# Kernel optimization log

Hardware: AMD Instinct MI355X
Metric: run time of the kernel (lower is better)

## Reference

```python
import math
import jax, jax.numpy as jnp
import numpy as np

N_HEAD = 16
HEAD_DIM = 128


def _rope(x, cos, sin):
    # x: (B,T,H,D); cos,sin: (T,1,D/2) broadcast over B,H
    d = x.shape[-1] // 2
    x1, x2 = x[..., :d], x[..., d:]
    return jnp.concatenate([x1 * cos + x2 * sin, -x1 * sin + x2 * cos], axis=-1)


def _rms_norm(x, eps=1e-6):
    return x * jax.lax.rsqrt(jnp.mean(x * x, axis=-1, keepdims=True) + eps)


def setup_inputs() -> dict:
    key = jax.random.key(0)
    ks = jax.random.split(key, 9)
    B, T, C = 2, 2048, 2048
    scale = 1.0 / math.sqrt(C)
    return {
        "x": jax.random.normal(ks[0], (B, T, C), jnp.float32),
        "ve": jax.random.normal(ks[1], (B, T, C), jnp.float32),
        "Wq": jax.random.normal(ks[2], (C, C), jnp.float32) * scale,
        "Wk": jax.random.normal(ks[3], (C, C), jnp.float32) * scale,
        "Wv": jax.random.normal(ks[4], (C, C), jnp.float32) * scale,
        "Wproj": jax.random.normal(ks[5], (C, C), jnp.float32) * scale,
        "Wgate": jax.random.normal(ks[6], (N_HEAD, 12), jnp.float32) * (1.0 / math.sqrt(12.0)),
        "cos": jax.random.uniform(ks[7], (T, 1, HEAD_DIM // 2), jnp.float32),
        "sin": jax.random.uniform(ks[8], (T, 1, HEAD_DIM // 2), jnp.float32),
        "window_left": 1024,
    }


def reference(x, ve, Wq, Wk, Wv, Wproj, Wgate, cos, sin, window_left):
    B, T, C = x.shape
    H, D = N_HEAD, HEAD_DIM

    # Linear projections (torch Linear: x @ W.T)
    q = (x @ Wq.T).reshape(B, T, H, D)
    k = (x @ Wk.T).reshape(B, T, H, D)
    v = (x @ Wv.T).reshape(B, T, H, D)

    # value-embedding gating (has_ve layer)
    gate = 3.0 * jax.nn.sigmoid(x[..., :12] @ Wgate.T)  # (B,T,H)
    v = v + gate[..., None] * ve.reshape(B, T, H, D)

    # rope + qk rms-norm * 1.2
    q = _rms_norm(_rope(q, cos, sin)) * 1.2
    k = _rms_norm(_rope(k, cos, sin)) * 1.2

    # windowed causal mask
    row = jnp.arange(T)[:, None]
    col = jnp.arange(T)[None, :]
    mask = row >= col
    if 0 < window_left < T:
        mask = mask & (row - col <= window_left)
    bias = jnp.where(mask, 0.0, -1e9).astype(x.dtype)  # (T,T)

    scale = 1.0 / math.sqrt(D)
    att = jnp.einsum("bqhd,bkhd->bhqk", q, k) * scale + bias[None, None]
    att = jax.nn.softmax(att, axis=-1)
    y = jnp.einsum("bhqk,bkhd->bqhd", att, v).reshape(B, T, H * D)
    return y @ Wproj.T
```

## Files before the change

### kernel.cpp

```cpp
#include <hip/hip_runtime.h>
#include <hip/hip_bf16.h>
#include <cstdint>

#define N_HEAD 16
#define HEAD_DIM 128

typedef __bf16 bf16;
typedef __bf16 bf16x8 __attribute__((ext_vector_type(8)));
typedef __bf16 bf16x4 __attribute__((ext_vector_type(4)));
typedef float f32x4 __attribute__((ext_vector_type(4)));

__device__ __forceinline__ void gload_lds16(const void* g, void* l) {
  auto gp = reinterpret_cast<const __attribute__((address_space(1))) char*>(
      reinterpret_cast<uintptr_t>(g));
  auto lp = reinterpret_cast<__attribute__((address_space(3))) char*>(
      reinterpret_cast<uintptr_t>(l));
  __builtin_amdgcn_global_load_lds(gp, lp, 16, 0, 0);
}

__global__ __launch_bounds__(256) void cvt_all(
    const float* __restrict__ x, const float* __restrict__ Wq,
    const float* __restrict__ Wk, const float* __restrict__ Wv,
    const float* __restrict__ Wp, bf16* __restrict__ xb,
    bf16* __restrict__ wqkv, bf16* __restrict__ wpb, int nx4, int nw4) {
  const int z = blockIdx.z;
  const float* in;
  bf16* out;
  int n4;
  if (z == 0)      { in = x;  out = xb;  n4 = nx4; }
  else if (z == 1) { in = Wq; out = wqkv;                     n4 = nw4; }
  else if (z == 2) { in = Wk; out = wqkv + (size_t)nw4 * 4;   n4 = nw4; }
  else if (z == 3) { in = Wv; out = wqkv + (size_t)nw4 * 8;   n4 = nw4; }
  else             { in = Wp; out = wpb;  n4 = nw4; }
  const int i = blockIdx.x * 256 + threadIdx.x;
  if (i >= n4) return;
  const float4 f = reinterpret_cast<const float4*>(in)[i];
  bf16x4 o;
  o.x = (bf16)f.x; o.y = (bf16)f.y; o.z = (bf16)f.z; o.w = (bf16)f.w;
  reinterpret_cast<bf16x4*>(out)[i] = o;
}

__global__ __launch_bounds__(512, 2) void gemm256(
    const bf16* __restrict__ A, const bf16* __restrict__ Bt,
    bf16* __restrict__ C, int M, int N, int K) {
  __shared__ __align__(16) char sA[2][32768];
  __shared__ __align__(16) char sB[2][32768];

  const int nwgy = M >> 8;
  const int nwg = gridDim.x;
  const int q8 = nwg >> 3;
  const int wgid = (blockIdx.x & 7) * q8 + (blockIdx.x >> 3);
  const int by = wgid % nwgy;
  const int bx = wgid / nwgy;

  const int tid = threadIdx.x;
  const int lane = tid & 63;
  const int wave = tid >> 6;
  const int wm = (wave >> 2) << 7;
  const int wn = (wave & 3) << 6;
  const int lr = lane & 15;
  const int lk16 = (lane >> 4) << 4;
  const int sx = (lr & 7) << 4;

  const bf16* Ab = A + (size_t)by * 256 * K;
  const bf16* Bb = Bt + (size_t)bx * 256 * K;

  int srow[2], scol[2];
#pragma unroll
  for (int pp = 0; pp < 2; ++pp) {
    const int o = pp * 8192 + tid * 16;
    srow[pp] = o >> 7;
    scol[pp] = (o & 127) ^ ((srow[pp] & 7) << 4);
  }

  auto stageA = [&](int buf, int half, int k0) {
#pragma unroll
    for (int pp = 0; pp < 2; ++pp)
      gload_lds16(Ab + (size_t)(half * 128 + srow[pp]) * K + k0 + (scol[pp] >> 1),
                  sA[buf] + half * 16384 + pp * 8192 + tid * 16);
  };
  auto stageB = [&](int buf, int half, int k0) {
#pragma unroll
    for (int pp = 0; pp < 2; ++pp)
      gload_lds16(Bb + (size_t)(half * 128 + srow[pp]) * K + k0 + (scol[pp] >> 1),
                  sB[buf] + half * 16384 + pp * 8192 + tid * 16);
  };

  f32x4 acc[8][4] = {};
  bf16x8 bF[4][2];

#define VMCNT4                                             \
  asm volatile("s_waitcnt vmcnt(4)" ::: "memory");         \
  __builtin_amdgcn_sched_barrier(0)
#define VMCNT0                                             \
  asm volatile("s_waitcnt vmcnt(0)" ::: "memory");         \
  __builtin_amdgcn_sched_barrier(0)

#define PHASE(BUF, P, STAGE, WAIT)                                             \
  {                                                                            \
    bf16x8 aF[2][2];                                                           \
    if (P == 0) {                                                              \
      _Pragma("unroll") for (int n = 0; n < 4; ++n)                            \
      _Pragma("unroll") for (int ks = 0; ks < 2; ++ks)                         \
        bF[n][ks] = *reinterpret_cast<const bf16x8*>(                          \
            sB[BUF] + (wn + n * 16 + lr) * 128 + ((ks * 64 + lk16) ^ sx));     \
    }                                                                          \
    _Pragma("unroll") for (int mi = 0; mi < 2; ++mi)                           \
    _Pragma("unroll") for (int ks = 0; ks < 2; ++ks)                           \
      aF[mi][ks] = *reinterpret_cast<const bf16x8*>(                           \
          sA[BUF] + (wm + (P * 2 + mi) * 16 + lr) * 128 +                      \
          ((ks * 64 + lk16) ^ sx));                                            \
    STAGE;                                                                     \
    WAIT;                                                                      \
    __builtin_amdgcn_s_barrier();                                              \
    __builtin_amdgcn_s_setprio(1);                                             \
    _Pragma("unroll") for (int ks = 0; ks < 2; ++ks)                           \
    _Pragma("unroll") for (int mi = 0; mi < 2; ++mi)                           \
    _Pragma("unroll") for (int n = 0; n < 4; ++n)                              \
      acc[P * 2 + mi][n] = __builtin_amdgcn_mfma_f32_16x16x32_bf16(            \
          aF[mi][ks], bF[n][ks], acc[P * 2 + mi][n], 0, 0, 0);                 \
    __builtin_amdgcn_s_setprio(0);                                             \
    __builtin_amdgcn_s_barrier();                                              \
  }

  const int nIt = K >> 7;

  stageB(0, 0, 0); stageB(0, 1, 0);
  stageA(0, 0, 0); stageA(0, 1, 0);
  stageB(1, 0, 64); stageB(1, 1, 64);
  VMCNT4;
  __builtin_amdgcn_s_barrier();

  int k0 = 0;
  for (int it = 0; it < nIt - 1; ++it, k0 += 128) {
    PHASE(0, 0, stageA(1, 0, k0 + 64), );
    PHASE(0, 1, stageA(1, 1, k0 + 64), );
    PHASE(0, 2, stageB(0, 0, k0 + 128), );
    PHASE(0, 3, stageB(0, 1, k0 + 128), VMCNT4);
    PHASE(1, 0, stageA(0, 0, k0 + 128), );
    PHASE(1, 1, stageA(0, 1, k0 + 128), );
    PHASE(1, 2, stageB(1, 0, k0 + 192), );
    PHASE(1, 3, stageB(1, 1, k0 + 192), VMCNT4);
  }
  PHASE(0, 0, stageA(1, 0, k0 + 64), );
  PHASE(0, 1, stageA(1, 1, k0 + 64), );
  PHASE(0, 2, , );
  PHASE(0, 3, , VMCNT0);
  PHASE(1, 0, , );
  PHASE(1, 1, , );
  PHASE(1, 2, , );
  PHASE(1, 3, , );
#undef PHASE
#undef VMCNT4
#undef VMCNT0

  const int orow = by * 256 + wm + (lane >> 4) * 4;
  const int ocol = bx * 256 + wn + lr;
#pragma unroll
  for (int m = 0; m < 8; ++m)
#pragma unroll
    for (int n = 0; n < 4; ++n)
#pragma unroll
      for (int r = 0; r < 4; ++r)
        C[(size_t)(orow + m * 16 + r) * N + (ocol + n * 16)] = (bf16)acc[m][n][r];
}

template <typename OutT>
__global__ __launch_bounds__(512, 2) void gemm128(
    const bf16* __restrict__ A, const bf16* __restrict__ Bt,
    OutT* __restrict__ C, int M, int Ncols, int K, int nOff) {
  __shared__ __align__(16) char sA[2][16384];
  __shared__ __align__(16) char sB[2][32768];

  const int nwgy = M >> 7;
  const int nwg = gridDim.x;
  const int q8 = nwg >> 3;
  const int wgid = (blockIdx.x & 7) * q8 + (blockIdx.x >> 3);
  const int by = wgid % nwgy;
  const int bx = wgid / nwgy;

  const int tid = threadIdx.x;
  const int lane = tid & 63;
  const int wave = tid >> 6;
  const int wn = wave << 5;
  const int lr = lane & 15;
  const int lk16 = (lane >> 4) << 4;
  const int sx = (lr & 7) << 4;

  const bf16* Ab = A + (size_t)by * 128 * K;
  const bf16* Bb = Bt + (size_t)(nOff + bx * 256) * K;

  int srow[2], scol[2];
#pragma unroll
  for (int pp = 0; pp < 2; ++pp) {
    const int o = pp * 8192 + tid * 16;
    srow[pp] = o >> 7;
    scol[pp] = (o & 127) ^ ((srow[pp] & 7) << 4);
  }

  auto stageB = [&](int buf, int half, int k0) {
#pragma unroll
    for (int pp = 0; pp < 2; ++pp)
      gload_lds16(Bb + (size_t)(half * 128 + srow[pp]) * K + k0 + (scol[pp] >> 1),
                  sB[buf] + half * 16384 + pp * 8192 + tid * 16);
  };
  auto stageA = [&](int buf, int half, int k0) {
    const int o = tid * 16;
    const int row = o >> 7;
    const int col = (o & 127) ^ ((row & 7) << 4);
    gload_lds16(Ab + (size_t)(half * 64 + row) * K + k0 + (col >> 1),
                sA[buf] + half * 8192 + o);
  };

  f32x4 acc[8][2] = {};
  bf16x8 bF[2][2];

#define WAITV(n)                                               \
  asm volatile("s_waitcnt vmcnt(" #n ")" ::: "memory");        \
  __builtin_amdgcn_sched_barrier(0)

#define PH128(BUF, P, STAGE, WAIT)                                             \
  {                                                                            \
    bf16x8 aF[2][2];                                                           \
    if (P == 0) {                                                              \
      _Pragma("unroll") for (int n = 0; n < 2; ++n)                            \
      _Pragma("unroll") for (int ks = 0; ks < 2; ++ks)                         \
        bF[n][ks] = *reinterpret_cast<const bf16x8*>(                          \
            sB[BUF] + (wn + n * 16 + lr) * 128 + ((ks * 64 + lk16) ^ sx));     \
    }                                                                          \
    _Pragma("unroll") for (int mi = 0; mi < 2; ++mi)                           \
    _Pragma("unroll") for (int ks = 0; ks < 2; ++ks)                           \
      aF[mi][ks] = *reinterpret_cast<const bf16x8*>(                           \
          sA[BUF] + ((P * 2 + mi) * 16 + lr) * 128 + ((ks * 64 + lk16) ^ sx)); \
    STAGE;                                                                     \
    WAIT;                                                                      \
    __builtin_amdgcn_s_barrier();                                              \
    __builtin_amdgcn_s_setprio(1);                                             \
    _Pragma("unroll") for (int ks = 0; ks < 2; ++ks)                           \
    _Pragma("unroll") for (int mi = 0; mi < 2; ++mi)                           \
    _Pragma("unroll") for (int n = 0; n < 2; ++n)                              \
      acc[P * 2 + mi][n] = __builtin_amdgcn_mfma_f32_16x16x32_bf16(            \
          aF[mi][ks], bF[n][ks], acc[P * 2 + mi][n], 0, 0, 0);                 \
    __builtin_amdgcn_s_setprio(0);                                             \
    __builtin_amdgcn_s_barrier();                                              \
  }

  const int nIt = K >> 7;

  stageB(0, 0, 0); stageB(0, 1, 0);
  stageA(0, 0, 0); stageA(0, 1, 0);
  stageB(1, 0, 64); stageB(1, 1, 64);
  stageA(1, 0, 64);
  WAITV(5);
  __builtin_amdgcn_s_barrier();

  int k0 = 0;
  for (int it = 0; it < nIt - 1; ++it, k0 += 128) {
    PH128(0, 0, stageA(1, 1, k0 + 64), );
    PH128(0, 1, stageB(0, 0, k0 + 128), WAITV(8));
    PH128(0, 2, (stageB(0, 1, k0 + 128), stageA(0, 0, k0 + 128)), );
    PH128(0, 3, , WAITV(6));
    PH128(1, 0, stageA(0, 1, k0 + 128), );
    PH128(1, 1, stageB(1, 0, k0 + 192), WAITV(8));
    PH128(1, 2, (stageB(1, 1, k0 + 192), stageA(1, 0, k0 + 192)), );
    PH128(1, 3, , WAITV(6));
  }
  PH128(0, 0, stageA(1, 1, k0 + 64), );
  PH128(0, 1, , WAITV(6));
  PH128(0, 2, , );
  PH128(0, 3, , WAITV(1));
  PH128(1, 0, , );
  PH128(1, 1, , WAITV(0));
  PH128(1, 2, , );
  PH128(1, 3, , );
#undef PH128
#undef WAITV

  const int orow = by * 128 + (lane >> 4) * 4;
  const int ocol = nOff + bx * 256 + wn + lr;
#pragma unroll
  for (int m = 0; m < 8; ++m)
#pragma unroll
    for (int n = 0; n < 2; ++n)
#pragma unroll
      for (int r = 0; r < 4; ++r)
        C[(size_t)(orow + m * 16 + r) * Ncols + (ocol + n * 16)] = (OutT)acc[m][n][r];
}

__global__ __launch_bounds__(256) void rope_rms(
    bf16* __restrict__ qkv, const float* __restrict__ cs,
    const float* __restrict__ sn, int T) {
  const int C = N_HEAD * HEAD_DIM;
  const int S = 3 * C;
  const int bt = blockIdx.x;
  const int t = bt % T;
  const int wave = threadIdx.x >> 6;
  const int lane = threadIdx.x & 63;
  const int h = blockIdx.y * 4 + wave;
  bf16* p = qkv + (size_t)bt * S + (blockIdx.z ? C : 0) + h * HEAD_DIM;
  const float oscale = blockIdx.z ? 1.2f : 0.15302091809294977f;
  const float c = cs[t * 64 + lane];
  const float s = sn[t * 64 + lane];
  const float x1 = (float)p[lane];
  const float x2 = (float)p[lane + 64];
  const float r1 = x1 * c + x2 * s;
  const float r2 = x2 * c - x1 * s;
  float ss = r1 * r1 + r2 * r2;
#pragma unroll
  for (int m = 1; m < 64; m <<= 1) ss += __shfl_xor(ss, m);
  const float sc = oscale * rsqrtf(ss * (1.0f / 128.0f) + 1e-6f);
  p[lane] = (bf16)(r1 * sc);
  p[lane + 64] = (bf16)(r2 * sc);
}

__global__ __launch_bounds__(256) void gate_transpose(
    const bf16* __restrict__ qkv, const float* __restrict__ x,
    const float* __restrict__ ve, const float* __restrict__ Wg,
    bf16* __restrict__ vT, int T) {
  const int C = N_HEAD * HEAD_DIM;
  const int S = 3 * C;
  const int t0 = blockIdx.x * 64;
  const int c0 = blockIdx.y * 64;
  const int b = blockIdx.z;
  const int h = c0 >> 7;

  __shared__ float gs[64];
  __shared__ __align__(16) bf16 tile[64][72];

  if (threadIdx.x < 64) {
    const float* xr = x + (size_t)(b * T + t0 + threadIdx.x) * C;
    float a = 0.f;
#pragma unroll
    for (int j = 0; j < 12; ++j) a += xr[j] * Wg[h * 12 + j];
    gs[threadIdx.x] = 3.f / (1.f + __expf(-a));
  }
  __syncthreads();

  {
    const int r = threadIdx.x >> 2;
    const int cc = (threadIdx.x & 3) * 16;
    const size_t vrow = (size_t)(b * T + t0 + r) * S + 2 * C + c0 + cc;
    const size_t erow = (size_t)(b * T + t0 + r) * C + c0 + cc;
    bf16x8 a0 = *reinterpret_cast<const bf16x8*>(qkv + vrow);
    bf16x8 a1 = *reinterpret_cast<const bf16x8*>(qkv + vrow + 8);
    const float g = gs[r];
    bf16x8 o0, o1;
#pragma unroll
    for (int i = 0; i < 8; ++i) o0[i] = (bf16)((float)a0[i] + g * ve[erow + i]);
#pragma unroll
    for (int i = 0; i < 8; ++i) o1[i] = (bf16)((float)a1[i] + g * ve[erow + 8 + i]);
    *reinterpret_cast<bf16x8*>(&tile[r][cc]) = o0;
    *reinterpret_cast<bf16x8*>(&tile[r][cc + 8]) = o1;
  }
  __syncthreads();
  {
    const int dr = threadIdx.x >> 2;
    const int tc = (threadIdx.x & 3) * 16;
    bf16x8 o0, o1;
#pragma unroll
    for (int i = 0; i < 8; ++i) o0[i] = tile[tc + i][dr];
#pragma unroll
    for (int i = 0; i < 8; ++i) o1[i] = tile[tc + 8 + i][dr];
    const size_t orow =
        ((size_t)((b * N_HEAD + h) * HEAD_DIM) + (c0 & 127) + dr) * T + t0 + tc;
    *reinterpret_cast<bf16x8*>(vT + orow) = o0;
    *reinterpret_cast<bf16x8*>(vT + orow + 8) = o1;
  }
}

__global__ __launch_bounds__(256, 2) void attn(
    const bf16* __restrict__ qkv, const bf16* __restrict__ vT,
    bf16* __restrict__ y, const int* __restrict__ wptr, int T, int B) {
  const int C = N_HEAD * HEAD_DIM;
  const int S = 3 * C;
  const int nq = T >> 7;
  const int ppx = (B * N_HEAD) >> 3;
  const int bid = blockIdx.x;
  const int xcd = bid & 7;
  const int sl = bid >> 3;
  const int pair = xcd * ppx + sl / nq;
  const int qi = sl % nq;
  const int b = pair / N_HEAD;
  const int h = pair % N_HEAD;
  const int qb = qi * 128;

  const int tid = threadIdx.x;
  const int wave = tid >> 6;
  const int lane = tid & 63;
  const int lm = lane & 15;
  const int quad = lane >> 4;

  const int w = wptr[0];
  const int W = (w > 0 && w < T) ? w : (1 << 30);

  __shared__ __align__(16) bf16 Ks[4][64][32];
  __shared__ __align__(16) bf16 Vs[2][128][32];
  __shared__ __align__(16) bf16 Pb[4][16][72];

  const bf16* kb = qkv + (size_t)b * T * S + C + (size_t)h * HEAD_DIM;
  const bf16* vb = vT + (size_t)((b * N_HEAD + h) * HEAD_DIM) * T;

  const int qt[2] = {qb + wave * 16, qb + 64 + wave * 16};
  bf16x8 qf[2][4];
#pragma unroll
  for (int t = 0; t < 2; ++t) {
    const bf16* qrow = qkv + (size_t)(b * T + qt[t] + lm) * S + h * HEAD_DIM;
#pragma unroll
    for (int c = 0; c < 4; ++c)
      qf[t][c] = *reinterpret_cast<const bf16x8*>(qrow + c * 32 + quad * 8);
  }

  float mrun[2] = {-1e30f, -1e30f}, lrun[2] = {0.f, 0.f};
  f32x4 oacc[2][8] = {};

  int kstart = qb - W;
  if (kstart < 0) kstart = 0;
  kstart &= ~63;
  const int kend = qb + 64;

  const int sr = tid >> 2;
  const int sc = (tid & 3) * 8;

  bf16x8 kpre[4], vpre[4];
  {
    const bf16* kr = kb + (size_t)(kstart + sr) * S + sc;
#pragma unroll
    for (int c = 0; c < 4; ++c)
      kpre[c] = *reinterpret_cast<const bf16x8*>(kr + c * 32);
#pragma unroll
    for (int c2 = 0; c2 < 2; ++c2)
#pragma unroll
      for (int i = 0; i < 2; ++i)
        vpre[c2 * 2 + i] = *reinterpret_cast<const bf16x8*>(
            vb + (size_t)(i * 64 + sr) * T + kstart + c2 * 32 + sc);
  }

  for (int kc = kstart; kc <= kend; kc += 64) {
    __syncthreads();
#pragma unroll
    for (int c = 0; c < 4; ++c)
      *reinterpret_cast<bf16x8*>(&Ks[c][sr][sc]) = kpre[c];
#pragma unroll
    for (int c2 = 0; c2 < 2; ++c2)
#pragma unroll
      for (int i = 0; i < 2; ++i)
        *reinterpret_cast<bf16x8*>(&Vs[c2][i * 64 + sr][sc]) = vpre[c2 * 2 + i];
    __syncthreads();

    if (kc + 64 <= kend) {
      const int kc2 = kc + 64;
      const bf16* kr = kb + (size_t)(kc2 + sr) * S + sc;
#pragma unroll
      for (int c = 0; c < 4; ++c)
        kpre[c] = *reinterpret_cast<const bf16x8*>(kr + c * 32);
#pragma unroll
      for (int c2 = 0; c2 < 2; ++c2)
#pragma unroll
        for (int i = 0; i < 2; ++i)
          vpre[c2 * 2 + i] = *reinterpret_cast<const bf16x8*>(
              vb + (size_t)(i * 64 + sr) * T + kc2 + c2 * 32 + sc);
    }

#pragma unroll
    for (int t = 0; t < 2; ++t) {
      const int q0 = qt[t];
      if (kc > q0 + 15 || kc + 63 < q0 - W) continue;
      const int qr = q0 + lm;

      f32x4 st[4] = {};
#pragma unroll
      for (int g = 0; g < 4; ++g)
#pragma unroll
        for (int c = 0; c < 4; ++c) {
          const bf16x8 kf =
              *reinterpret_cast<const bf16x8*>(&Ks[c][g * 16 + lm][quad * 8]);
          st[g] = __builtin_amdgcn_mfma_f32_16x16x32_bf16(kf, qf[t][c], st[g], 0, 0, 0);
        }
      float mx = -1e30f;
#pragma unroll
      for (int g = 0; g < 4; ++g)
#pragma unroll
        for (int r = 0; r < 4; ++r) {
          const int key = kc + g * 16 + quad * 4 + r;
          const bool valid = (key <= qr) && (qr - key <= W);
          st[g][r] = valid ? st[g][r] : -1e30f;
          mx = fmaxf(mx, st[g][r]);
        }
      mx = fmaxf(mx, __shfl_xor(mx, 16));
      mx = fmaxf(mx, __shfl_xor(mx, 32));
      const float mnew = fmaxf(mrun[t], mx);
      const float alpha = __builtin_amdgcn_exp2f(mrun[t] - mnew);
      mrun[t] = mnew;
      float rs = 0.f;
#pragma unroll
      for (int g = 0; g < 4; ++g) {
        bf16x4 pk;
#pragma unroll
        for (int r = 0; r < 4; ++r) {
          const float p = __builtin_amdgcn_exp2f(st[g][r] - mnew);
          rs += p;
          pk[r] = (bf16)p;
        }
        *reinterpret_cast<bf16x4*>(&Pb[wave][lm][g * 16 + quad * 4]) = pk;
      }
      rs += __shfl_xor(rs, 16);
      rs += __shfl_xor(rs, 32);
      lrun[t] = lrun[t] * alpha + rs;
#pragma unroll
      for (int dc = 0; dc < 8; ++dc)
#pragma unroll
        for (int r = 0; r < 4; ++r) oacc[t][dc][r] *= alpha;
#pragma unroll
      for (int c2 = 0; c2 < 2; ++c2) {
        const bf16x8 pf =
            *reinterpret_cast<const bf16x8*>(&Pb[wave][lm][c2 * 32 + quad * 8]);
#pragma unroll
        for (int dc = 0; dc < 8; ++dc) {
          const bf16x8 vf =
              *reinterpret_cast<const bf16x8*>(&Vs[c2][dc * 16 + lm][quad * 8]);
          oacc[t][dc] = __builtin_amdgcn_mfma_f32_16x16x32_bf16(vf, pf, oacc[t][dc], 0, 0, 0);
        }
      }
    }
  }

#pragma unroll
  for (int t = 0; t < 2; ++t) {
    const float inv = 1.f / lrun[t];
    bf16* yr = y + (size_t)(b * T + qt[t] + lm) * C + h * HEAD_DIM;
#pragma unroll
    for (int dc = 0; dc < 8; ++dc) {
      bf16x4 o;
#pragma unroll
      for (int r = 0; r < 4; ++r) o[r] = (bf16)(oacc[t][dc][r] * inv);
      *reinterpret_cast<bf16x4*>(yr + dc * 16 + quad * 4) = o;
    }
  }
}

extern "C" void kernel_launch(void* const* d_in, const int* in_sizes, int n_in,
                              void* d_out, int out_size, void* d_ws, size_t ws_size,
                              hipStream_t stream) {
  const float* x  = (const float*)d_in[0];
  const float* ve = (const float*)d_in[1];
  const float* Wq = (const float*)d_in[2];
  const float* Wk = (const float*)d_in[3];
  const float* Wv = (const float*)d_in[4];
  const float* Wp = (const float*)d_in[5];
  const float* Wg = (const float*)d_in[6];
  const float* cs = (const float*)d_in[7];
  const float* sn = (const float*)d_in[8];
  const int*   wl = (const int*)d_in[9];
  float* out = (float*)d_out;

  const int C = N_HEAD * HEAD_DIM;
  const int T = in_sizes[7] / (HEAD_DIM / 2);
  const int B = in_sizes[0] / (T * C);
  const int M = B * T;

  bf16* xb   = (bf16*)d_ws;
  bf16* wqkv = xb   + (size_t)M * C;
  bf16* wpb  = wqkv + (size_t)3 * C * C;
  bf16* qkv  = wpb  + (size_t)C * C;
  bf16* ybuf = qkv  + (size_t)3 * M * C;
  bf16* vTb  = xb;

  const int nx4 = M * C / 4, nw4 = C * C / 4;
  cvt_all<<<dim3((nx4 + 255) / 256, 1, 5), 256, 0, stream>>>(
      x, Wq, Wk, Wv, Wp, xb, wqkv, wpb, nx4, nw4);

  gemm256<<<dim3((M / 256) * 16), 512, 0, stream>>>(xb, wqkv, qkv, M, 3 * C, C);
  gemm128<bf16><<<dim3((M / 128) * 8), 512, 0, stream>>>(
      xb, wqkv, qkv, M, 3 * C, C, 2 * C);

  rope_rms<<<dim3(M, N_HEAD / 4, 2), 256, 0, stream>>>(qkv, cs, sn, T);
  gate_transpose<<<dim3(T / 64, C / 64, B), 256, 0, stream>>>(qkv, x, ve, Wg, vTb, T);
  attn<<<dim3(B * N_HEAD * (T / 128)), 256, 0, stream>>>(qkv, vTb, ybuf, wl, T, B);

  gemm128<float><<<dim3((M / 128) * (C / 256)), 512, 0, stream>>>(
      ybuf, wpb, out, M, C, C, 0);
}
```

Before: 395.8 us.

## Shrink attention query tile, swizzle LDS, lazy rescale, vectorize rope and gate loads

The attention kernel now gives each block 64 queries instead of 128, doubling the grid and raising the occupancy hint to 4 blocks per CU. It also switches K/V/P shared memory to XOR-swizzled layouts to reduce bank conflicts and skips the output rescale when the running max does not change. Separately, rope_rms processes each head with 16 lanes using vector loads, and gate_transpose loads ve with float4. The smaller query tile means each K/V tile is reused by fewer queries, so global traffic for K/V goes up.

```diff
diff --git a/kernel.cpp b/kernel.cpp
--- a/kernel.cpp
+++ b/kernel.cpp
@@ -292,25 +292,44 @@
     const float* __restrict__ sn, int T) {
   const int C = N_HEAD * HEAD_DIM;
   const int S = 3 * C;
-  const int bt = blockIdx.x;
+  const int r = blockIdx.x * 16 + (threadIdx.x >> 4);
+  const int l = threadIdx.x & 15;
+  const int bt = r >> 5;
+  const int rem = r & 31;
+  const int z = rem >> 4;
+  const int h = rem & 15;
   const int t = bt % T;
-  const int wave = threadIdx.x >> 6;
-  const int lane = threadIdx.x & 63;
-  const int h = blockIdx.y * 4 + wave;
-  bf16* p = qkv + (size_t)bt * S + (blockIdx.z ? C : 0) + h * HEAD_DIM;
-  const float oscale = blockIdx.z ? 1.2f : 0.15302091809294977f;
-  const float c = cs[t * 64 + lane];
-  const float s = sn[t * 64 + lane];
-  const float x1 = (float)p[lane];
-  const float x2 = (float)p[lane + 64];
-  const float r1 = x1 * c + x2 * s;
-  const float r2 = x2 * c - x1 * s;
-  float ss = r1 * r1 + r2 * r2;
-#pragma unroll
-  for (int m = 1; m < 64; m <<= 1) ss += __shfl_xor(ss, m);
+  bf16* p = qkv + (size_t)bt * S + z * C + h * HEAD_DIM;
+  const float oscale = z ? 1.2f : 0.15302091809294977f;
+
+  const float4 c4 = *reinterpret_cast<const float4*>(cs + t * 64 + l * 4);
+  const float4 s4 = *reinterpret_cast<const float4*>(sn + t * 64 + l * 4);
+  const float cj[4] = {c4.x, c4.y, c4.z, c4.w};
+  const float sj[4] = {s4.x, s4.y, s4.z, s4.w};
+  const bf16x4 xa = *reinterpret_cast<const bf16x4*>(p + l * 4);
+  const bf16x4 xb = *reinterpret_cast<const bf16x4*>(p + 64 + l * 4);
+
+  float r1[4], r2[4];
+  float ss = 0.f;
+#pragma unroll
+  for (int j = 0; j < 4; ++j) {
+    const float x1 = (float)xa[j];
+    const float x2 = (float)xb[j];
+    r1[j] = x1 * cj[j] + x2 * sj[j];
+    r2[j] = x2 * cj[j] - x1 * sj[j];
+    ss += r1[j] * r1[j] + r2[j] * r2[j];
+  }
+#pragma unroll
+  for (int m = 1; m < 16; m <<= 1) ss += __shfl_xor(ss, m);
   const float sc = oscale * rsqrtf(ss * (1.0f / 128.0f) + 1e-6f);
-  p[lane] = (bf16)(r1 * sc);
-  p[lane + 64] = (bf16)(r2 * sc);
+  bf16x4 o1, o2;
+#pragma unroll
+  for (int j = 0; j < 4; ++j) {
+    o1[j] = (bf16)(r1[j] * sc);
+    o2[j] = (bf16)(r2[j] * sc);
+  }
+  *reinterpret_cast<bf16x4*>(p + l * 4) = o1;
+  *reinterpret_cast<bf16x4*>(p + 64 + l * 4) = o2;
 }
 
 __global__ __launch_bounds__(256) void gate_transpose(
@@ -343,12 +362,16 @@
     const size_t erow = (size_t)(b * T + t0 + r) * C + c0 + cc;
     bf16x8 a0 = *reinterpret_cast<const bf16x8*>(qkv + vrow);
     bf16x8 a1 = *reinterpret_cast<const bf16x8*>(qkv + vrow + 8);
+    const float4* vep = reinterpret_cast<const float4*>(ve + erow);
+    const float4 e0 = vep[0], e1 = vep[1], e2 = vep[2], e3 = vep[3];
+    const float ev[16] = {e0.x, e0.y, e0.z, e0.w, e1.x, e1.y, e1.z, e1.w,
+                          e2.x, e2.y, e2.z, e2.w, e3.x, e3.y, e3.z, e3.w};
     const float g = gs[r];
     bf16x8 o0, o1;
 #pragma unroll
-    for (int i = 0; i < 8; ++i) o0[i] = (bf16)((float)a0[i] + g * ve[erow + i]);
-#pragma unroll
-    for (int i = 0; i < 8; ++i) o1[i] = (bf16)((float)a1[i] + g * ve[erow + 8 + i]);
+    for (int i = 0; i < 8; ++i) o0[i] = (bf16)((float)a0[i] + g * ev[i]);
+#pragma unroll
+    for (int i = 0; i < 8; ++i) o1[i] = (bf16)((float)a1[i] + g * ev[8 + i]);
     *reinterpret_cast<bf16x8*>(&tile[r][cc]) = o0;
     *reinterpret_cast<bf16x8*>(&tile[r][cc + 8]) = o1;
   }
@@ -368,12 +391,12 @@
   }
 }
 
-__global__ __launch_bounds__(256, 2) void attn(
+__global__ __launch_bounds__(256, 4) void attn(
     const bf16* __restrict__ qkv, const bf16* __restrict__ vT,
     bf16* __restrict__ y, const int* __restrict__ wptr, int T, int B) {
   const int C = N_HEAD * HEAD_DIM;
   const int S = 3 * C;
-  const int nq = T >> 7;
+  const int nq = T >> 6;
   const int ppx = (B * N_HEAD) >> 3;
   const int bid = blockIdx.x;
   const int xcd = bid & 7;
@@ -382,99 +405,97 @@
   const int qi = sl % nq;
   const int b = pair / N_HEAD;
   const int h = pair % N_HEAD;
-  const int qb = qi * 128;
+  const int qb = qi * 64;
 
   const int tid = threadIdx.x;
   const int wave = tid >> 6;
   const int lane = tid & 63;
   const int lm = lane & 15;
   const int quad = lane >> 4;
+  const int lmw = (lm & 7) << 3;
 
   const int w = wptr[0];
   const int W = (w > 0 && w < T) ? w : (1 << 30);
 
-  __shared__ __align__(16) bf16 Ks[4][64][32];
-  __shared__ __align__(16) bf16 Vs[2][128][32];
-  __shared__ __align__(16) bf16 Pb[4][16][72];
+  __shared__ __align__(16) bf16 Ks[64][128];
+  __shared__ __align__(16) bf16 Vs[128][64];
+  __shared__ __align__(16) bf16 Pb[4][16][64];
 
   const bf16* kb = qkv + (size_t)b * T * S + C + (size_t)h * HEAD_DIM;
   const bf16* vb = vT + (size_t)((b * N_HEAD + h) * HEAD_DIM) * T;
 
-  const int qt[2] = {qb + wave * 16, qb + 64 + wave * 16};
-  bf16x8 qf[2][4];
-#pragma unroll
-  for (int t = 0; t < 2; ++t) {
-    const bf16* qrow = qkv + (size_t)(b * T + qt[t] + lm) * S + h * HEAD_DIM;
+  const int qt = qb + wave * 16;
+  const int qr = qt + lm;
+  bf16x8 qf[4];
+  {
+    const bf16* qrow = qkv + (size_t)(b * T + qr) * S + h * HEAD_DIM;
 #pragma unroll
     for (int c = 0; c < 4; ++c)
-      qf[t][c] = *reinterpret_cast<const bf16x8*>(qrow + c * 32 + quad * 8);
-  }
-
-  float mrun[2] = {-1e30f, -1e30f}, lrun[2] = {0.f, 0.f};
-  f32x4 oacc[2][8] = {};
+      qf[c] = *reinterpret_cast<const bf16x8*>(qrow + c * 32 + quad * 8);
+  }
+
+  float mrun = -1e30f, lrun = 0.f;
+  f32x4 oacc[8] = {};
 
   int kstart = qb - W;
   if (kstart < 0) kstart = 0;
   kstart &= ~63;
-  const int kend = qb + 64;
+  const int kend = qb;
 
   const int sr = tid >> 2;
-  const int sc = (tid & 3) * 8;
+  const int s4 = (tid & 3) * 8;
+  const int swz = (sr & 7) << 3;
 
   bf16x8 kpre[4], vpre[4];
   {
-    const bf16* kr = kb + (size_t)(kstart + sr) * S + sc;
+    const bf16* kr = kb + (size_t)(kstart + sr) * S;
 #pragma unroll
     for (int c = 0; c < 4; ++c)
-      kpre[c] = *reinterpret_cast<const bf16x8*>(kr + c * 32);
+      kpre[c] = *reinterpret_cast<const bf16x8*>(kr + c * 32 + s4);
 #pragma unroll
     for (int c2 = 0; c2 < 2; ++c2)
 #pragma unroll
       for (int i = 0; i < 2; ++i)
         vpre[c2 * 2 + i] = *reinterpret_cast<const bf16x8*>(
-            vb + (size_t)(i * 64 + sr) * T + kstart + c2 * 32 + sc);
+            vb + (size_t)(i * 64 + sr) * T + kstart + c2 * 32 + s4);
   }
 
   for (int kc = kstart; kc <= kend; kc += 64) {
     __syncthreads();
 #pragma unroll
     for (int c = 0; c < 4; ++c)
-      *reinterpret_cast<bf16x8*>(&Ks[c][sr][sc]) = kpre[c];
+      *reinterpret_cast<bf16x8*>(&Ks[sr][(c * 32 + s4) ^ swz]) = kpre[c];
 #pragma unroll
     for (int c2 = 0; c2 < 2; ++c2)
 #pragma unroll
       for (int i = 0; i < 2; ++i)
-        *reinterpret_cast<bf16x8*>(&Vs[c2][i * 64 + sr][sc]) = vpre[c2 * 2 + i];
+        *reinterpret_cast<bf16x8*>(&Vs[i * 64 + sr][(c2 * 32 + s4) ^ swz]) =
+            vpre[c2 * 2 + i];
     __syncthreads();
 
     if (kc + 64 <= kend) {
       const int kc2 = kc + 64;
-      const bf16* kr = kb + (size_t)(kc2 + sr) * S + sc;
+      const bf16* kr = kb + (size_t)(kc2 + sr) * S;
 #pragma unroll
       for (int c = 0; c < 4; ++c)
-        kpre[c] = *reinterpret_cast<const bf16x8*>(kr + c * 32);
+        kpre[c] = *reinterpret_cast<const bf16x8*>(kr + c * 32 + s4);
 #pragma unroll
       for (int c2 = 0; c2 < 2; ++c2)
 #pragma unroll
         for (int i = 0; i < 2; ++i)
           vpre[c2 * 2 + i] = *reinterpret_cast<const bf16x8*>(
-              vb + (size_t)(i * 64 + sr) * T + kc2 + c2 * 32 + sc);
+              vb + (size_t)(i * 64 + sr) * T + kc2 + c2 * 32 + s4);
     }
 
-#pragma unroll
-    for (int t = 0; t < 2; ++t) {
-      const int q0 = qt[t];
-      if (kc > q0 + 15 || kc + 63 < q0 - W) continue;
-      const int qr = q0 + lm;
-
+    if (kc <= qt + 15 && kc + 63 >= qt - W) {
       f32x4 st[4] = {};
 #pragma unroll
       for (int g = 0; g < 4; ++g)
 #pragma unroll
         for (int c = 0; c < 4; ++c) {
-          const bf16x8 kf =
-              *reinterpret_cast<const bf16x8*>(&Ks[c][g * 16 + lm][quad * 8]);
-          st[g] = __builtin_amdgcn_mfma_f32_16x16x32_bf16(kf, qf[t][c], st[g], 0, 0, 0);
+          const bf16x8 kf = *reinterpret_cast<const bf16x8*>(
+              &Ks[g * 16 + lm][(c * 32 + quad * 8) ^ lmw]);
+          st[g] = __builtin_amdgcn_mfma_f32_16x16x32_bf16(kf, qf[c], st[g], 0, 0, 0);
         }
       float mx = -1e30f;
 #pragma unroll
@@ -482,57 +503,60 @@
 #pragma unroll
         for (int r = 0; r < 4; ++r) {
           const int key = kc + g * 16 + quad * 4 + r;
-          const bool valid = (key <= qr) && (qr - key <= W);
+          const bool valid = (unsigned)(qr - key) <= (unsigned)W;
           st[g][r] = valid ? st[g][r] : -1e30f;
           mx = fmaxf(mx, st[g][r]);
         }
       mx = fmaxf(mx, __shfl_xor(mx, 16));
       mx = fmaxf(mx, __shfl_xor(mx, 32));
-      const float mnew = fmaxf(mrun[t], mx);
-      const float alpha = __builtin_amdgcn_exp2f(mrun[t] - mnew);
-      mrun[t] = mnew;
+      float alpha = 1.f;
+      if (!__all(mx <= mrun)) {
+        const float mnew = fmaxf(mrun, mx);
+        alpha = __builtin_amdgcn_exp2f(mrun - mnew);
+        mrun = mnew;
+#pragma unroll
+        for (int dc = 0; dc < 8; ++dc)
+#pragma unroll
+          for (int r = 0; r < 4; ++r) oacc[dc][r] *= alpha;
+      }
       float rs = 0.f;
 #pragma unroll
       for (int g = 0; g < 4; ++g) {
         bf16x4 pk;
 #pragma unroll
         for (int r = 0; r < 4; ++r) {
-          const float p = __builtin_amdgcn_exp2f(st[g][r] - mnew);
+          const float p = __builtin_amdgcn_exp2f(st[g][r] - mrun);
           rs += p;
           pk[r] = (bf16)p;
         }
-        *reinterpret_cast<bf16x4*>(&Pb[wave][lm][g * 16 + quad * 4]) = pk;
+        *reinterpret_cast<bf16x4*>(
+            &Pb[wave][lm][((g * 16 + (quad >> 1) * 8) ^ lmw) + (quad & 1) * 4]) = pk;
       }
       rs += __shfl_xor(rs, 16);
       rs += __shfl_xor(rs, 32);
-      lrun[t] = lrun[t] * alpha + rs;
-#pragma unroll
-      for (int dc = 0; dc < 8; ++dc)
-#pragma unroll
-        for (int r = 0; r < 4; ++r) oacc[t][dc][r] *= alpha;
+      lrun = lrun * alpha + rs;
 #pragma unroll
       for (int c2 = 0; c2 < 2; ++c2) {
-        const bf16x8 pf =
-            *reinterpret_cast<const bf16x8*>(&Pb[wave][lm][c2 * 32 + quad * 8]);
+        const bf16x8 pf = *reinterpret_cast<const bf16x8*>(
+            &Pb[wave][lm][(c2 * 32 + quad * 8) ^ lmw]);
 #pragma unroll
         for (int dc = 0; dc < 8; ++dc) {
-          const bf16x8 vf =
-              *reinterpret_cast<const bf16x8*>(&Vs[c2][dc * 16 + lm][quad * 8]);
-          oacc[t][dc] = __builtin_amdgcn_mfma_f32_16x16x32_bf16(vf, pf, oacc[t][dc], 0, 0, 0);
+          const bf16x8 vf = *reinterpret_cast<const bf16x8*>(
+              &Vs[dc * 16 + lm][(c2 * 32 + quad * 8) ^ lmw]);
+          oacc[dc] = __builtin_amdgcn_mfma_f32_16x16x32_bf16(vf, pf, oacc[dc], 0, 0, 0);
         }
       }
     }
   }
 
-#pragma unroll
-  for (int t = 0; t < 2; ++t) {
-    const float inv = 1.f / lrun[t];
-    bf16* yr = y + (size_t)(b * T + qt[t] + lm) * C + h * HEAD_DIM;
+  {
+    const float inv = 1.f / lrun;
+    bf16* yr = y + (size_t)(b * T + qr) * C + h * HEAD_DIM;
 #pragma unroll
     for (int dc = 0; dc < 8; ++dc) {
       bf16x4 o;
 #pragma unroll
-      for (int r = 0; r < 4; ++r) o[r] = (bf16)(oacc[t][dc][r] * inv);
+      for (int r = 0; r < 4; ++r) o[r] = (bf16)(oacc[dc][r] * inv);
       *reinterpret_cast<bf16x4*>(yr + dc * 16 + quad * 4) = o;
     }
   }
@@ -573,9 +597,9 @@
   gemm128<bf16><<<dim3((M / 128) * 8), 512, 0, stream>>>(
       xb, wqkv, qkv, M, 3 * C, C, 2 * C);
 
-  rope_rms<<<dim3(M, N_HEAD / 4, 2), 256, 0, stream>>>(qkv, cs, sn, T);
+  rope_rms<<<dim3(M * 2), 256, 0, stream>>>(qkv, cs, sn, T);
   gate_transpose<<<dim3(T / 64, C / 64, B), 256, 0, stream>>>(qkv, x, ve, Wg, vTb, T);
-  attn<<<dim3(B * N_HEAD * (T / 128)), 256, 0, stream>>>(qkv, vTb, ybuf, wl, T, B);
+  attn<<<dim3(B * N_HEAD * (T / 64)), 256, 0, stream>>>(qkv, vTb, ybuf, wl, T, B);
 
   gemm128<float><<<dim3((M / 128) * (C / 256)), 512, 0, stream>>>(
       ybuf, wpb, out, M, C, C, 0);
```

New measurement: 420.7 us. 1.06x slower.
